# Kernel tuning notes

Hardware: AMD Instinct MI355X
Metric: run time of the kernel (lower is better)

Reference implementation:

```python
import jax, jax.numpy as jnp
import numpy as np
from jax import lax

B, C, H, W = 4096, 10, 30, 30
NCOL = C - 1                      # non-background colors 1..9
_pi, _pj = np.triu_indices(NCOL, 1)  # lexicographic (i<j) pair order, matches the python double loop
PI = jnp.asarray(_pi); PJ = jnp.asarray(_pj)
NPAIR = int(_pi.shape[0])         # 36
W_TRANSFORM, W_EXACT, W_AFFINE, W_ROT, W_REFL, W_GEO, W_EDGE, W_CBAL = 0.2, 7.0, 0.4, 0.3, 0.3, 0.5, 0.3, 0.2
GAMMA = 1.4


def setup_inputs() -> dict:
    key = jax.random.key(0)
    ks = jax.random.split(key, 6)
    pred = jax.random.normal(ks[0], (B, C, H, W), jnp.float32)
    tidx = jax.random.randint(ks[1], (B, H, W), 0, C)
    target = jnp.transpose(jax.nn.one_hot(tidx, C, dtype=jnp.float32), (0, 3, 1, 2))
    iidx = jax.random.randint(ks[2], (B, H, W), 0, C)
    input_grid = jnp.transpose(jax.nn.one_hot(iidx, C, dtype=jnp.float32), (0, 3, 1, 2))
    theta = 0.1 * jax.random.normal(ks[3], (B, 2, 3), jnp.float32)
    rot = jax.random.normal(ks[4], (B, 8), jnp.float32)
    refl = jax.random.normal(ks[5], (B, 4), jnp.float32)
    return {"pred_output": pred, "target_output": target, "input_grid": input_grid,
            "theta": theta, "rotation_logits": rot, "reflection_logits": refl}


def _detect_edges(idx):
    # idx: [B,H,W] int; pixel is an edge if it differs from any h/w neighbor
    dh = idx[:, 1:, :] != idx[:, :-1, :]
    dw = idx[:, :, 1:] != idx[:, :, :-1]
    e = jnp.pad(dh, ((0, 0), (1, 0), (0, 0))) | jnp.pad(dh, ((0, 0), (0, 1), (0, 0)))
    e = e | jnp.pad(dw, ((0, 0), (0, 0), (1, 0))) | jnp.pad(dw, ((0, 0), (0, 0), (0, 1)))
    return e


def _entropy_mean(logits):
    lp = jax.nn.log_softmax(logits, axis=1)
    return (-(jnp.exp(lp) * lp).sum(axis=1)).mean()


def _sobel(idx_f):
    sx = jnp.array([[-1., 0., 1.], [-2., 0., 2.], [-1., 0., 1.]], jnp.float32).reshape(1, 1, 3, 3)
    sy = jnp.array([[-1., -2., -1.], [0., 0., 0.], [1., 2., 1.]], jnp.float32).reshape(1, 1, 3, 3)
    x = idx_f[:, None]  # [B,1,H,W]
    dn = ('NCHW', 'OIHW', 'NCHW')
    ex = lax.conv_general_dilated(x, sx, (1, 1), ((1, 1), (1, 1)), dimension_numbers=dn)
    ey = lax.conv_general_dilated(x, sy, (1, 1), ((1, 1), (1, 1)), dimension_numbers=dn)
    return jnp.sqrt(ex * ex + ey * ey)


def _centers(grid):
    # grid: [H,W] int -> per-color (1..9) center of mass and presence
    cols = jnp.arange(1, C)
    mask = (grid[None] == cols[:, None, None]).astype(jnp.float32)  # [9,H,W]
    cnt = mask.sum((1, 2))
    ys = jnp.arange(H, dtype=jnp.float32)[:, None]
    xs = jnp.arange(W, dtype=jnp.float32)[None, :]
    cy = (mask * ys).sum((1, 2)) / jnp.maximum(cnt, 1.0)
    cx = (mask * xs).sum((1, 2)) / jnp.maximum(cnt, 1.0)
    return cy, cx, cnt > 0


def _compact_dists(cy, cx, present):
    # distances for all 36 color pairs, compacted so valid pairs occupy
    # the leading slots in the same lexicographic order as the torch loops
    d = jnp.sqrt((cy[PI] - cy[PJ]) ** 2 + (cx[PI] - cx[PJ]) ** 2)
    v = present[PI] & present[PJ]
    rank = jnp.cumsum(v.astype(jnp.int32)) - 1
    slot = jnp.where(v, rank, NPAIR)          # dump invalid pairs in scratch slot
    compact = jnp.zeros(NPAIR + 1, jnp.float32).at[slot].set(d)
    return compact[:NPAIR], v.sum()


def _geo_sample(pidx, tidx):
    cyp, cxp, prp = _centers(pidx)
    cyt, cxt, prt = _centers(tidx)
    dp, n_p = _compact_dists(cyp, cxp, prp)
    dt, n_t = _compact_dists(cyt, cxt, prt)
    m = jnp.minimum(n_p, n_t)                 # min_len truncation
    use = jnp.arange(NPAIR) < m
    sq = jnp.where(use, (dp - dt) ** 2, 0.0)
    return jnp.where(m > 0, sq.sum() / jnp.maximum(m, 1).astype(jnp.float32), 0.0)


def _components(pred, target, inp, theta, rot, refl):
    tidx = jnp.argmax(target, axis=1)
    pidx = jnp.argmax(pred, axis=1)
    iidx = jnp.argmax(inp, axis=1)
    # spatial focal CE with edge-weighted pixels
    lp = jax.nn.log_softmax(pred, axis=1)
    ce = -jnp.take_along_axis(lp, tidx[:, None], axis=1)[:, 0]  # [B,H,W]
    pt = jnp.exp(-ce)
    sw = jnp.where(_detect_edges(tidx), 1.5, 1.0)
    spatial_focal = ((1.0 - pt) ** GAMMA * ce * sw).mean()
    # exact match bonus / copy penalty
    exact = jnp.all(pidx == tidx, axis=(1, 2)).astype(jnp.float32)
    exact_count = exact.sum()
    exact_bonus = -exact.mean() * W_EXACT
    copy = jnp.all(pidx == iidx, axis=(1, 2)).astype(jnp.float32)
    transform = copy.mean() * W_TRANSFORM
    # affine regularization on theta
    scale_reg = jnp.sqrt((theta[:, :2, :2] ** 2).sum((1, 2)))
    trans_reg = jnp.sqrt((theta[:, :, 2] ** 2).sum(1))
    affine = (scale_reg.mean() + 0.1 * trans_reg.mean()) * W_AFFINE
    rotation = _entropy_mean(rot) * W_ROT
    reflection = _entropy_mean(refl) * W_REFL
    # geometric color-center consistency (vmapped over batch)
    geo = jax.vmap(_geo_sample)(pidx, tidx).sum() / B * W_GEO
    # sobel edge MSE on argmax indices
    pe = _sobel(pidx.astype(jnp.float32))
    te = _sobel(tidx.astype(jnp.float32))
    edge = jnp.mean((pe - te) ** 2) * W_EDGE
    # color balance
    pc = jax.nn.softmax(pred, axis=1).sum((2, 3))
    tc = target.sum((2, 3))
    pc = pc / (pc.sum(1, keepdims=True) + 1e-8)
    tc = tc / (tc.sum(1, keepdims=True) + 1e-8)
    cbal = jnp.mean((pc - tc) ** 2) * W_CBAL
    total = (spatial_focal + transform + affine + rotation + reflection
             + geo + edge + cbal + exact_bonus)
    return (total, spatial_focal, transform, exact_bonus, exact_count,
            affine, rotation, reflection, geo, edge, cbal)


def reference(pred_output, target_output, input_grid, theta, rotation_logits, reflection_logits):
    return _components(pred_output, target_output, input_grid, theta,
                       rotation_logits, reflection_logits)
```

## Files before the change

### kernel.cpp

```cpp
#include <hip/hip_runtime.h>
#include <stdint.h>

#define B_   4096
#define C_   10
#define H_   30
#define W_   30
#define HW_  900
#define NCOL_ 9
#define NPART 9


__device__ __forceinline__ float entropyN(const float* __restrict__ x, int n) {
    float m = x[0];
    for (int i = 1; i < n; ++i) m = fmaxf(m, x[i]);
    float se = 0.f;
    for (int i = 0; i < n; ++i) se += __expf(x[i] - m);
    float lse = m + __logf(se);
    float ent = 0.f;
    for (int i = 0; i < n; ++i) { float lp = x[i] - lse; ent -= __expf(lp) * lp; }
    return ent;
}


__global__ __launch_bounds__(64) void zero_out_k(float* out, int n) {
    int i = threadIdx.x;
    if (i < n) out[i] = 0.f;
}

__global__ __launch_bounds__(256) void loss_main(
    const float* __restrict__ pred, const float* __restrict__ target,
    const float* __restrict__ inp,  const float* __restrict__ theta,
    const float* __restrict__ rotl, const float* __restrict__ refl,
    float* __restrict__ partials ,
    float* __restrict__ out)
{
    __shared__ uint8_t s_t[33 * 32];
    __shared__ uint8_t s_p[33 * 32];
    __shared__ __align__(16) float s_cef[30 * 36];
    __shared__ unsigned long long s_ctr[2][NCOL_];
    __shared__ float s_wred[4][16];
    __shared__ float s_dp[36], s_dt[36];

    const int t = threadIdx.x;
    const int b = blockIdx.x;
    const size_t base = (size_t)b * (C_ * HW_);

    float pc[C_];
#pragma unroll
    for (int c = 0; c < C_; ++c) pc[c] = 0.f;
    float exact_f = 1.f, copy_f = 1.f;

    if (t < 225) {
        const int p0 = 4 * t;
        float v[C_][4];
        float vt[4]  = {0.f, 0.f, 0.f, 0.f};
        float tif[4] = {0.f, 0.f, 0.f, 0.f};
        float iif[4] = {0.f, 0.f, 0.f, 0.f};
#pragma unroll
        for (int c = 0; c < C_; ++c) {
            float4 tf = *reinterpret_cast<const float4*>(target + base + (size_t)c * HW_ + p0);
            float4 pf = *reinterpret_cast<const float4*>(pred   + base + (size_t)c * HW_ + p0);
            float4 gf = *reinterpret_cast<const float4*>(inp    + base + (size_t)c * HW_ + p0);
            v[c][0] = pf.x; v[c][1] = pf.y; v[c][2] = pf.z; v[c][3] = pf.w;
            const float fc = (float)c;
            vt[0] = fmaf(tf.x, pf.x, vt[0]); vt[1] = fmaf(tf.y, pf.y, vt[1]);
            vt[2] = fmaf(tf.z, pf.z, vt[2]); vt[3] = fmaf(tf.w, pf.w, vt[3]);
            tif[0] = fmaf(tf.x, fc, tif[0]); tif[1] = fmaf(tf.y, fc, tif[1]);
            tif[2] = fmaf(tf.z, fc, tif[2]); tif[3] = fmaf(tf.w, fc, tif[3]);
            iif[0] = fmaf(gf.x, fc, iif[0]); iif[1] = fmaf(gf.y, fc, iif[1]);
            iif[2] = fmaf(gf.z, fc, iif[2]); iif[3] = fmaf(gf.w, fc, iif[3]);
        }
        int h = p0 / 30;
        int w = p0 - 30 * h;
#pragma unroll
        for (int j = 0; j < 4; ++j) {
            const int ti = (int)tif[j];
            const int ii = (int)iif[j];
            float pm = v[0][j]; int pi = 0;
            float se = 0.f;
#pragma unroll
            for (int c = 0; c < C_; ++c) {
                float raw = v[c][j];
                if (c > 0 && raw > pm) { pm = raw; pi = c; }
                float e = __expf(raw);
                v[c][j] = e;
                se += e;
            }
            const float inv = __builtin_amdgcn_rcpf(se);
#pragma unroll
            for (int c = 0; c < C_; ++c) pc[c] = fmaf(v[c][j], inv, pc[c]);
            const float ce = __logf(se) - vt[j];

            s_t[(h + 1) * 32 + (w + 1)] = (uint8_t)ti;
            s_p[(h + 1) * 32 + (w + 1)] = (uint8_t)pi;
            s_cef[36 * h + w] = ce;
            if (pi != ti) exact_f = 0.f;
            if (pi != ii) copy_f = 0.f;
            if (++w == 30) { w = 0; ++h; }
        }
    } else {
        const int z = t - 225;
        for (int k = z; k < 32; k += 31) {
            const int g = k >> 4, r = (k >> 3) & 1, dw = k & 7;
            uint32_t* pb = (uint32_t*)((g ? s_p : s_t) + (r ? 31 * 32 : 0));
            pb[dw] = 0u;
        }
        for (int k = z; k < 120; k += 31) {
            const int g = (k >= 60);
            const int kk = k - 60 * g;
            const int r = 1 + (kk >> 1);
            const int cp = (kk & 1) ? 31 : 0;
            (g ? s_p : s_t)[r * 32 + cp] = 0;
        }
        for (int k = z; k < 2 * NCOL_; k += 31) ((unsigned long long*)s_ctr)[k] = 0ull;
    }
    __syncthreads();

    float focal = 0.f, edg = 0.f;
    if (t < 240) {
        const int h = t >> 3, wq = t & 7;
        const int w0 = 4 * wq;
        const int npx = (w0 < 28) ? 4 : 2;

        const uint32_t* tr0 = (const uint32_t*)(s_t + 32 * h);
        const uint32_t* tr1 = (const uint32_t*)(s_t + 32 * (h + 1));
        const uint32_t* tr2 = (const uint32_t*)(s_t + 32 * (h + 2));
        const uint32_t* pr0 = (const uint32_t*)(s_p + 32 * h);
        const uint32_t* pr1 = (const uint32_t*)(s_p + 32 * (h + 1));
        const uint32_t* pr2 = (const uint32_t*)(s_p + 32 * (h + 2));

        uint32_t td[3][2] = {{tr0[wq], tr0[wq + 1]}, {tr1[wq], tr1[wq + 1]}, {tr2[wq], tr2[wq + 1]}};
        uint32_t pd[3][2] = {{pr0[wq], pr0[wq + 1]}, {pr1[wq], pr1[wq + 1]}, {pr2[wq], pr2[wq + 1]}};
        const float4 cef = *reinterpret_cast<const float4*>(s_cef + 36 * h + w0);
        const float cearr[4] = {cef.x, cef.y, cef.z, cef.w};

        int tb[3][6], pb[3][6];
#pragma unroll
        for (int r = 0; r < 3; ++r) {
            const uint32_t d0t = td[r][0], d1t = td[r][1];
            tb[r][0] = d0t & 255; tb[r][1] = (d0t >> 8) & 255; tb[r][2] = (d0t >> 16) & 255;
            tb[r][3] = d0t >> 24; tb[r][4] = d1t & 255; tb[r][5] = (d1t >> 8) & 255;
            const uint32_t d0p = pd[r][0], d1p = pd[r][1];
            pb[r][0] = d0p & 255; pb[r][1] = (d0p >> 8) & 255; pb[r][2] = (d0p >> 16) & 255;
            pb[r][3] = d0p >> 24; pb[r][4] = d1p & 255; pb[r][5] = (d1p >> 8) & 255;
        }
        int s1t[6], s2t[6], s1p[6], s2p[6];
#pragma unroll
        for (int j = 0; j < 6; ++j) {
            s1t[j] = tb[0][j] + 2 * tb[1][j] + tb[2][j];
            s2t[j] = tb[2][j] - tb[0][j];
            s1p[j] = pb[0][j] + 2 * pb[1][j] + pb[2][j];
            s2p[j] = pb[2][j] - pb[0][j];
        }
#pragma unroll
        for (int k = 0; k < 4; ++k) {
            if (k < npx) {
                const int w = w0 + k;
                const int tv = tb[1][k + 1], pv = pb[1][k + 1];
                const bool eg = (h > 0  && tb[0][k + 1] != tv) ||
                                (h < 29 && tb[2][k + 1] != tv) ||
                                (w > 0  && tb[1][k]     != tv) ||
                                (w < 29 && tb[1][k + 2] != tv);
                const float ce = cearr[k];
                const float pt = __expf(-ce);
                const float omt = fmaxf(1.f - pt, 0.f);
                focal += __powf(omt, 1.4f) * ce * (eg ? 1.5f : 1.0f);

                const int ext = s1t[k + 2] - s1t[k];
                const int eyt = s2t[k] + 2 * s2t[k + 1] + s2t[k + 2];
                const int exq = s1p[k + 2] - s1p[k];
                const int eyq = s2p[k] + 2 * s2p[k + 1] + s2p[k + 2];
                const float mt = sqrtf((float)(ext * ext + eyt * eyt));
                const float mp = sqrtf((float)(exq * exq + eyq * eyq));
                const float dd = mp - mt;
                edg += dd * dd;

                const unsigned long long add =
                    (1ull << 42) | ((unsigned long long)(unsigned)h << 21) | (unsigned)w;
                if (tv > 0) atomicAdd(&s_ctr[1][tv - 1], add);
                if (pv > 0) atomicAdd(&s_ctr[0][pv - 1], add);
            }
        }
    }

    float vals[14];
    vals[0] = focal; vals[1] = edg;
#pragma unroll
    for (int c = 0; c < C_; ++c) vals[2 + c] = pc[c];
    vals[12] = exact_f; vals[13] = copy_f;
#pragma unroll
    for (int off = 32; off > 0; off >>= 1) {
#pragma unroll
        for (int k = 0; k < 12; ++k) vals[k] += __shfl_down(vals[k], off);
        vals[12] = fminf(vals[12], __shfl_down(vals[12], off));
        vals[13] = fminf(vals[13], __shfl_down(vals[13], off));
    }
    const int wid = t >> 6, lane = t & 63;
    if (lane == 0) {
#pragma unroll
        for (int k = 0; k < 14; ++k) s_wred[wid][k] = vals[k];
    }
    __syncthreads();

    if (t == 0) {
        float r[14];
#pragma unroll
        for (int k = 0; k < 14; ++k) r[k] = s_wred[0][k];
        for (int w2 = 1; w2 < 4; ++w2) {
#pragma unroll
            for (int k = 0; k < 12; ++k) r[k] += s_wred[w2][k];
            r[12] = fminf(r[12], s_wred[w2][12]);
            r[13] = fminf(r[13], s_wred[w2][13]);
        }

        float cyp[NCOL_], cxp[NCOL_], cyt[NCOL_], cxt[NCOL_];
        bool  prp[NCOL_], prt[NCOL_];
        int   tcnt[NCOL_];
        int   tsum = 0;
#pragma unroll
        for (int k = 0; k < NCOL_; ++k) {
            unsigned long long q0 = s_ctr[0][k];
            int sx0 = (int)(q0 & 0x1FFFFF), sy0 = (int)((q0 >> 21) & 0x1FFFFF), c0 = (int)(q0 >> 42);
            prp[k] = (c0 > 0);
            float d0 = fmaxf((float)c0, 1.f);
            cyp[k] = (float)sy0 / d0; cxp[k] = (float)sx0 / d0;
            unsigned long long q1 = s_ctr[1][k];
            int sx1 = (int)(q1 & 0x1FFFFF), sy1 = (int)((q1 >> 21) & 0x1FFFFF), c1 = (int)(q1 >> 42);
            prt[k] = (c1 > 0);
            float d1 = fmaxf((float)c1, 1.f);
            cyt[k] = (float)sy1 / d1; cxt[k] = (float)sx1 / d1;
            tcnt[k] = c1; tsum += c1;
        }

        int np = 0, nt = 0;
#pragma unroll
        for (int i = 0; i < NCOL_; ++i) {
#pragma unroll
            for (int j = i + 1; j < NCOL_; ++j) {
                if (prp[i] && prp[j]) {
                    float dy = cyp[i] - cyp[j], dx = cxp[i] - cxp[j];
                    s_dp[np++] = sqrtf(dy * dy + dx * dx);
                }
                if (prt[i] && prt[j]) {
                    float dy = cyt[i] - cyt[j], dx = cxt[i] - cxt[j];
                    s_dt[nt++] = sqrtf(dy * dy + dx * dx);
                }
            }
        }
        int mm = np < nt ? np : nt;
        float geo_b = 0.f;
        for (int k = 0; k < mm; ++k) { float d = s_dp[k] - s_dt[k]; geo_b += d * d; }
        geo_b = (mm > 0) ? geo_b / (float)mm : 0.f;

        float pcs = 0.f;
#pragma unroll
        for (int c = 0; c < C_; ++c) pcs += r[2 + c];
        float cb = 0.f;
        const float tdenom = 900.f + 1e-8f;
        {
            float pcn0 = r[2] / (pcs + 1e-8f);
            float tcn0 = (float)(HW_ - tsum) / tdenom;
            float d = pcn0 - tcn0; cb += d * d;
        }
#pragma unroll
        for (int c = 1; c < C_; ++c) {
            float pcn = r[2 + c] / (pcs + 1e-8f);
            float tcn = (float)tcnt[c - 1] / tdenom;
            float d = pcn - tcn;
            cb += d * d;
        }

        const float* th = theta + (size_t)b * 6;
        float sreg = sqrtf(th[0]*th[0] + th[1]*th[1] + th[3]*th[3] + th[4]*th[4]);
        float treg = sqrtf(th[2]*th[2] + th[5]*th[5]);
        float ent_r = entropyN(rotl + (size_t)b * 8, 8);
        float ent_f = entropyN(refl + (size_t)b * 4, 4);

        float res[NPART];
        res[0] = r[0];
        res[1] = r[12];
        res[2] = r[13];
        res[3] = sreg + 0.1f * treg;
        res[4] = ent_r;
        res[5] = ent_f;
        res[6] = geo_b;
        res[7] = r[1];
        res[8] = cb;

        if (partials) {
            float* pp = partials + (size_t)b * NPART;
#pragma unroll
            for (int k = 0; k < NPART; ++k) pp[k] = res[k];
        } else {
            atomicAdd(&out[1],  res[0]);
            atomicAdd(&out[2],  res[2]);
            atomicAdd(&out[4],  res[1]);
            atomicAdd(&out[5],  res[3]);
            atomicAdd(&out[6],  res[4]);
            atomicAdd(&out[7],  res[5]);
            atomicAdd(&out[8],  res[6]);
            atomicAdd(&out[9],  res[7]);
            atomicAdd(&out[10], res[8]);
        }
    }
}

__device__ __forceinline__ void write_final(float* out,
    double focal_s, double exact_s, double copy_s, double aff_s,
    double rot_s, double refl_s, double geo_s, double edge_s, double cbal_s)
{
    const double invB = 1.0 / (double)B_;
    float focal      = (float)(focal_s / ((double)B_ * (double)HW_));
    float transform  = (float)(copy_s * invB * 0.2);
    float exact_cnt  = (float)exact_s;
    float exact_bns  = (float)(-(exact_s * invB) * 7.0);
    float affine     = (float)(aff_s * invB * 0.4);
    float rotation   = (float)(rot_s * invB * 0.3);
    float reflection = (float)(refl_s * invB * 0.3);
    float geo        = (float)(geo_s * invB * 0.5);
    float edge       = (float)(edge_s / ((double)B_ * (double)HW_) * 0.3);
    float cbal       = (float)(cbal_s / ((double)B_ * (double)C_) * 0.2);
    out[0] = focal + transform + affine + rotation + reflection + geo + edge + cbal + exact_bns;
    out[1] = focal; out[2] = transform; out[3] = exact_bns; out[4] = exact_cnt;
    out[5] = affine; out[6] = rotation; out[7] = reflection; out[8] = geo;
    out[9] = edge; out[10] = cbal;
}

__global__ __launch_bounds__(256) void reduce_partials(
    const float* __restrict__ partials, float* __restrict__ out)
{
    __shared__ double sh[256][NPART];
    const int t = threadIdx.x;
    double acc[NPART];
#pragma unroll
    for (int k = 0; k < NPART; ++k) acc[k] = 0.0;
    for (int b = t; b < B_; b += 256) {
        const float* pp = partials + (size_t)b * NPART;
#pragma unroll
        for (int k = 0; k < NPART; ++k) acc[k] += (double)pp[k];
    }
#pragma unroll
    for (int k = 0; k < NPART; ++k) sh[t][k] = acc[k];
    __syncthreads();
    for (int s = 128; s > 0; s >>= 1) {
        if (t < s) {
#pragma unroll
            for (int k = 0; k < NPART; ++k) sh[t][k] += sh[t + s][k];
        }
        __syncthreads();
    }
    if (t == 0) {
        write_final(out, sh[0][0], sh[0][1], sh[0][2], sh[0][3],
                    sh[0][4], sh[0][5], sh[0][6], sh[0][7], sh[0][8]);
    }
}

__global__ void finalize_atomic(float* out) {
    if (threadIdx.x == 0) {
        write_final(out, (double)out[1], (double)out[4], (double)out[2], (double)out[5],
                    (double)out[6], (double)out[7], (double)out[8], (double)out[9],
                    (double)out[10]);
    }
}


extern "C" void kernel_launch(void* const* d_in, const int* in_sizes, int n_in,
                              void* d_out, int out_size, void* d_ws, size_t ws_size,
                              hipStream_t stream) {
    const float* pred   = (const float*)d_in[0];
    const float* target = (const float*)d_in[1];
    const float* inp    = (const float*)d_in[2];
    const float* theta  = (const float*)d_in[3];
    const float* rotl   = (const float*)d_in[4];
    const float* refl   = (const float*)d_in[5];
    float* out = (float*)d_out;

    const size_t need = (size_t)B_ * NPART * sizeof(float);
    if (d_ws != nullptr && ws_size >= need) {
        loss_main<<<B_, 256, 0, stream>>>(pred, target, inp, theta, rotl, refl,
                                          (float*)d_ws, out);
        reduce_partials<<<1, 256, 0, stream>>>((const float*)d_ws, out);
    } else {
        zero_out_k<<<1, 64, 0, stream>>>(out, out_size);
        loss_main<<<B_, 256, 0, stream>>>(pred, target, inp, theta, rotl, refl,
                                          nullptr, out);
        finalize_atomic<<<1, 1, 0, stream>>>(out);
    }
}
```

Baseline: 103.8 us.

## Parallelize per-block epilogue across lanes and hoist small-input work to idle threads

The serial single-thread epilogue is split up. Center decoding now runs on 18 threads. The 36 pairwise geo distances are computed one per lane of a wavefront and compacted with ballot/popcount before a shuffle reduction. Theta regularization and the rotation/reflection entropies move to otherwise idle threads before the first barrier, and pred/target loads are issued as batched float4 arrays to raise memory-level parallelism. Launch bounds now request 4 blocks per CU. The cost is an extra __syncthreads and higher register pressure from holding 20 float4 values.

```diff
diff --git a/kernel.cpp b/kernel.cpp
--- a/kernel.cpp
+++ b/kernel.cpp
@@ -27,7 +27,7 @@
     if (i < n) out[i] = 0.f;
 }
 
-__global__ __launch_bounds__(256) void loss_main(
+__global__ __launch_bounds__(256, 4) void loss_main(
     const float* __restrict__ pred, const float* __restrict__ target,
     const float* __restrict__ inp,  const float* __restrict__ theta,
     const float* __restrict__ rotl, const float* __restrict__ refl,
@@ -40,6 +40,10 @@
     __shared__ unsigned long long s_ctr[2][NCOL_];
     __shared__ float s_wred[4][16];
     __shared__ float s_dp[36], s_dt[36];
+    __shared__ float s_cy[2][NCOL_], s_cx[2][NCOL_];
+    __shared__ int   s_pr[2][NCOL_];
+    __shared__ int   s_tcnt[NCOL_];
+    __shared__ float s_small[4];
 
     const int t = threadIdx.x;
     const int b = blockIdx.x;
@@ -52,16 +56,27 @@
 
     if (t < 225) {
         const int p0 = 4 * t;
-        float v[C_][4];
+        const float* pp = pred   + base + p0;
+        const float* tp = target + base + p0;
+        const float* gp = inp    + base + p0;
+
+        float4 pfv[C_];
+#pragma unroll
+        for (int c = 0; c < C_; ++c)
+            pfv[c] = *reinterpret_cast<const float4*>(pp + c * HW_);
+        float4 tfv[C_];
+#pragma unroll
+        for (int c = 0; c < C_; ++c)
+            tfv[c] = *reinterpret_cast<const float4*>(tp + c * HW_);
+
         float vt[4]  = {0.f, 0.f, 0.f, 0.f};
         float tif[4] = {0.f, 0.f, 0.f, 0.f};
         float iif[4] = {0.f, 0.f, 0.f, 0.f};
 #pragma unroll
         for (int c = 0; c < C_; ++c) {
-            float4 tf = *reinterpret_cast<const float4*>(target + base + (size_t)c * HW_ + p0);
-            float4 pf = *reinterpret_cast<const float4*>(pred   + base + (size_t)c * HW_ + p0);
-            float4 gf = *reinterpret_cast<const float4*>(inp    + base + (size_t)c * HW_ + p0);
-            v[c][0] = pf.x; v[c][1] = pf.y; v[c][2] = pf.z; v[c][3] = pf.w;
+            float4 gf = *reinterpret_cast<const float4*>(gp + c * HW_);
+            const float4 tf = tfv[c];
+            const float4 pf = pfv[c];
             const float fc = (float)c;
             vt[0] = fmaf(tf.x, pf.x, vt[0]); vt[1] = fmaf(tf.y, pf.y, vt[1]);
             vt[2] = fmaf(tf.z, pf.z, vt[2]); vt[3] = fmaf(tf.w, pf.w, vt[3]);
@@ -70,25 +85,28 @@
             iif[0] = fmaf(gf.x, fc, iif[0]); iif[1] = fmaf(gf.y, fc, iif[1]);
             iif[2] = fmaf(gf.z, fc, iif[2]); iif[3] = fmaf(gf.w, fc, iif[3]);
         }
+
         int h = p0 / 30;
         int w = p0 - 30 * h;
 #pragma unroll
         for (int j = 0; j < 4; ++j) {
             const int ti = (int)tif[j];
             const int ii = (int)iif[j];
-            float pm = v[0][j]; int pi = 0;
+            const float* pj = (const float*)&pfv[0];
+            float pm = pj[j]; int pi = 0;
             float se = 0.f;
+            float ex[C_];
 #pragma unroll
             for (int c = 0; c < C_; ++c) {
-                float raw = v[c][j];
+                const float raw = ((const float*)&pfv[c])[j];
                 if (c > 0 && raw > pm) { pm = raw; pi = c; }
                 float e = __expf(raw);
-                v[c][j] = e;
+                ex[c] = e;
                 se += e;
             }
             const float inv = __builtin_amdgcn_rcpf(se);
 #pragma unroll
-            for (int c = 0; c < C_; ++c) pc[c] = fmaf(v[c][j], inv, pc[c]);
+            for (int c = 0; c < C_; ++c) pc[c] = fmaf(ex[c], inv, pc[c]);
             const float ce = __logf(se) - vt[j];
 
             s_t[(h + 1) * 32 + (w + 1)] = (uint8_t)ti;
@@ -98,21 +116,30 @@
             if (pi != ii) copy_f = 0.f;
             if (++w == 30) { w = 0; ++h; }
         }
-    } else {
+    } else if (t < 252) {
         const int z = t - 225;
-        for (int k = z; k < 32; k += 31) {
+        for (int k = z; k < 32; k += 27) {
             const int g = k >> 4, r = (k >> 3) & 1, dw = k & 7;
             uint32_t* pb = (uint32_t*)((g ? s_p : s_t) + (r ? 31 * 32 : 0));
             pb[dw] = 0u;
         }
-        for (int k = z; k < 120; k += 31) {
+        for (int k = z; k < 120; k += 27) {
             const int g = (k >= 60);
             const int kk = k - 60 * g;
             const int r = 1 + (kk >> 1);
             const int cp = (kk & 1) ? 31 : 0;
             (g ? s_p : s_t)[r * 32 + cp] = 0;
         }
-        for (int k = z; k < 2 * NCOL_; k += 31) ((unsigned long long*)s_ctr)[k] = 0ull;
+        for (int k = z; k < 2 * NCOL_; k += 27) ((unsigned long long*)s_ctr)[k] = 0ull;
+    } else if (t == 252) {
+        s_small[0] = entropyN(rotl + (size_t)b * 8, 8);
+    } else if (t == 253) {
+        s_small[1] = entropyN(refl + (size_t)b * 4, 4);
+    } else if (t == 254) {
+        const float* th = theta + (size_t)b * 6;
+        float sreg = sqrtf(th[0]*th[0] + th[1]*th[1] + th[3]*th[3] + th[4]*th[4]);
+        float treg = sqrtf(th[2]*th[2] + th[5]*th[5]);
+        s_small[2] = sreg + 0.1f * treg;
     }
     __syncthreads();
 
@@ -202,105 +229,105 @@
     }
     __syncthreads();
 
-    if (t == 0) {
-        float r[14];
-#pragma unroll
-        for (int k = 0; k < 14; ++k) r[k] = s_wred[0][k];
-        for (int w2 = 1; w2 < 4; ++w2) {
-#pragma unroll
-            for (int k = 0; k < 12; ++k) r[k] += s_wred[w2][k];
-            r[12] = fminf(r[12], s_wred[w2][12]);
-            r[13] = fminf(r[13], s_wred[w2][13]);
-        }
-
-        float cyp[NCOL_], cxp[NCOL_], cyt[NCOL_], cxt[NCOL_];
-        bool  prp[NCOL_], prt[NCOL_];
-        int   tcnt[NCOL_];
-        int   tsum = 0;
-#pragma unroll
-        for (int k = 0; k < NCOL_; ++k) {
-            unsigned long long q0 = s_ctr[0][k];
-            int sx0 = (int)(q0 & 0x1FFFFF), sy0 = (int)((q0 >> 21) & 0x1FFFFF), c0 = (int)(q0 >> 42);
-            prp[k] = (c0 > 0);
-            float d0 = fmaxf((float)c0, 1.f);
-            cyp[k] = (float)sy0 / d0; cxp[k] = (float)sx0 / d0;
-            unsigned long long q1 = s_ctr[1][k];
-            int sx1 = (int)(q1 & 0x1FFFFF), sy1 = (int)((q1 >> 21) & 0x1FFFFF), c1 = (int)(q1 >> 42);
-            prt[k] = (c1 > 0);
-            float d1 = fmaxf((float)c1, 1.f);
-            cyt[k] = (float)sy1 / d1; cxt[k] = (float)sx1 / d1;
-            tcnt[k] = c1; tsum += c1;
-        }
-
-        int np = 0, nt = 0;
-#pragma unroll
-        for (int i = 0; i < NCOL_; ++i) {
-#pragma unroll
-            for (int j = i + 1; j < NCOL_; ++j) {
-                if (prp[i] && prp[j]) {
-                    float dy = cyp[i] - cyp[j], dx = cxp[i] - cxp[j];
-                    s_dp[np++] = sqrtf(dy * dy + dx * dx);
-                }
-                if (prt[i] && prt[j]) {
-                    float dy = cyt[i] - cyt[j], dx = cxt[i] - cxt[j];
-                    s_dt[nt++] = sqrtf(dy * dy + dx * dx);
-                }
-            }
-        }
-        int mm = np < nt ? np : nt;
-        float geo_b = 0.f;
-        for (int k = 0; k < mm; ++k) { float d = s_dp[k] - s_dt[k]; geo_b += d * d; }
-        geo_b = (mm > 0) ? geo_b / (float)mm : 0.f;
-
-        float pcs = 0.f;
-#pragma unroll
-        for (int c = 0; c < C_; ++c) pcs += r[2 + c];
-        float cb = 0.f;
-        const float tdenom = 900.f + 1e-8f;
-        {
-            float pcn0 = r[2] / (pcs + 1e-8f);
-            float tcn0 = (float)(HW_ - tsum) / tdenom;
-            float d = pcn0 - tcn0; cb += d * d;
-        }
-#pragma unroll
-        for (int c = 1; c < C_; ++c) {
-            float pcn = r[2 + c] / (pcs + 1e-8f);
-            float tcn = (float)tcnt[c - 1] / tdenom;
-            float d = pcn - tcn;
-            cb += d * d;
-        }
-
-        const float* th = theta + (size_t)b * 6;
-        float sreg = sqrtf(th[0]*th[0] + th[1]*th[1] + th[3]*th[3] + th[4]*th[4]);
-        float treg = sqrtf(th[2]*th[2] + th[5]*th[5]);
-        float ent_r = entropyN(rotl + (size_t)b * 8, 8);
-        float ent_f = entropyN(refl + (size_t)b * 4, 4);
-
-        float res[NPART];
-        res[0] = r[0];
-        res[1] = r[12];
-        res[2] = r[13];
-        res[3] = sreg + 0.1f * treg;
-        res[4] = ent_r;
-        res[5] = ent_f;
-        res[6] = geo_b;
-        res[7] = r[1];
-        res[8] = cb;
-
-        if (partials) {
-            float* pp = partials + (size_t)b * NPART;
-#pragma unroll
-            for (int k = 0; k < NPART; ++k) pp[k] = res[k];
-        } else {
-            atomicAdd(&out[1],  res[0]);
-            atomicAdd(&out[2],  res[2]);
-            atomicAdd(&out[4],  res[1]);
-            atomicAdd(&out[5],  res[3]);
-            atomicAdd(&out[6],  res[4]);
-            atomicAdd(&out[7],  res[5]);
-            atomicAdd(&out[8],  res[6]);
-            atomicAdd(&out[9],  res[7]);
-            atomicAdd(&out[10], res[8]);
+    if (t < 18) {
+        const int g = (t >= 9);
+        const int k = t - 9 * g;
+        const unsigned long long q = s_ctr[g][k];
+        const int sx = (int)(q & 0x1FFFFF), sy = (int)((q >> 21) & 0x1FFFFF), cn = (int)(q >> 42);
+        const float dn = fmaxf((float)cn, 1.f);
+        s_cy[g][k] = (float)sy / dn;
+        s_cx[g][k] = (float)sx / dn;
+        s_pr[g][k] = (cn > 0);
+        if (g) s_tcnt[k] = cn;
+    }
+    __syncthreads();
+
+    if (t < 64) {
+        const int l = t;
+        const int i = (l >= 8) + (l >= 15) + (l >= 21) + (l >= 26) +
+                      (l >= 30) + (l >= 33) + (l >= 35);
+        const int j = l - (i * (17 - i)) / 2 + i + 1;
+        bool vp = false, vtp = false;
+        float dp = 0.f, dt = 0.f;
+        if (l < 36) {
+            vp  = s_pr[0][i] && s_pr[0][j];
+            vtp = s_pr[1][i] && s_pr[1][j];
+            float dyp = s_cy[0][i] - s_cy[0][j], dxp = s_cx[0][i] - s_cx[0][j];
+            dp = sqrtf(dyp * dyp + dxp * dxp);
+            float dyt = s_cy[1][i] - s_cy[1][j], dxt = s_cx[1][i] - s_cx[1][j];
+            dt = sqrtf(dyt * dyt + dxt * dxt);
+        }
+        const unsigned long long mp_mask = __ballot(vp);
+        const unsigned long long mt_mask = __ballot(vtp);
+        const unsigned long long below = (1ull << l) - 1ull;
+        if (vp)  s_dp[__popcll(mp_mask & below)] = dp;
+        if (vtp) s_dt[__popcll(mt_mask & below)] = dt;
+        const int np = (int)__popcll(mp_mask);
+        const int nt = (int)__popcll(mt_mask);
+        const int mm = np < nt ? np : nt;
+        float term = 0.f;
+        if (l < mm) { float d = s_dp[l] - s_dt[l]; term = d * d; }
+#pragma unroll
+        for (int off = 32; off > 0; off >>= 1) term += __shfl_down(term, off);
+
+        if (t == 0) {
+            const float geo_b = (mm > 0) ? term / (float)mm : 0.f;
+
+            float r[14];
+#pragma unroll
+            for (int k = 0; k < 14; ++k) r[k] = s_wred[0][k];
+            for (int w2 = 1; w2 < 4; ++w2) {
+#pragma unroll
+                for (int k = 0; k < 12; ++k) r[k] += s_wred[w2][k];
+                r[12] = fminf(r[12], s_wred[w2][12]);
+                r[13] = fminf(r[13], s_wred[w2][13]);
+            }
+
+            float pcs = 0.f;
+#pragma unroll
+            for (int c = 0; c < C_; ++c) pcs += r[2 + c];
+            const float ipcs = 1.f / (pcs + 1e-8f);
+            int tsum = 0;
+#pragma unroll
+            for (int k = 0; k < NCOL_; ++k) tsum += s_tcnt[k];
+            float cb = 0.f;
+            const float itd = 1.f / (900.f + 1e-8f);
+            {
+                float d = r[2] * ipcs - (float)(HW_ - tsum) * itd;
+                cb += d * d;
+            }
+#pragma unroll
+            for (int c = 1; c < C_; ++c) {
+                float d = r[2 + c] * ipcs - (float)s_tcnt[c - 1] * itd;
+                cb += d * d;
+            }
+
+            float res[NPART];
+            res[0] = r[0];
+            res[1] = r[12];
+            res[2] = r[13];
+            res[3] = s_small[2];
+            res[4] = s_small[0];
+            res[5] = s_small[1];
+            res[6] = geo_b;
+            res[7] = r[1];
+            res[8] = cb;
+
+            if (partials) {
+                float* pw = partials + (size_t)b * NPART;
+#pragma unroll
+                for (int k = 0; k < NPART; ++k) pw[k] = res[k];
+            } else {
+                atomicAdd(&out[1],  res[0]);
+                atomicAdd(&out[2],  res[2]);
+                atomicAdd(&out[4],  res[1]);
+                atomicAdd(&out[5],  res[3]);
+                atomicAdd(&out[6],  res[4]);
+                atomicAdd(&out[7],  res[5]);
+                atomicAdd(&out[8],  res[6]);
+                atomicAdd(&out[9],  res[7]);
+                atomicAdd(&out[10], res[8]);
+            }
         }
     }
 }
```

Result: faster. 94.75 us (-8.8%).
